# Kernel optimization log

Measured on AMD Instinct MI355X. Metric: run time of the kernel, lower is better.

Reference implementation:

```python
import jax, jax.numpy as jnp
import numpy as np

K_REP = 8
K_SMOOTH = 16
W_CHAMFER, W_REP, W_COV, W_SMOOTH = 1.0, 0.1, 0.2, 0.05
REP_THRESHOLD = 0.005


def setup_inputs() -> dict:
    key = jax.random.key(0)
    k1, k2, k3 = jax.random.split(key, 3)
    pred = jax.random.normal(k1, (4, 4096, 3), dtype=jnp.float32)
    gt = jax.random.normal(k2, (4, 4096, 3), dtype=jnp.float32)
    partial = jax.random.normal(k3, (4, 2048, 3), dtype=jnp.float32)
    return {"pred": pred, "gt": gt, "partial": partial}


def pairwise_dist(a, b):
    # a: [B,M,3], b: [B,N,3] -> Euclidean distances [B,M,N] (torch.cdist)
    sq = (jnp.sum(a * a, -1)[:, :, None] + jnp.sum(b * b, -1)[:, None, :]
          - 2.0 * jnp.einsum('bmd,bnd->bmn', a, b))
    sq = jnp.maximum(sq, 0.0)
    safe = jnp.where(sq > 1e-12, sq, 1.0)  # avoid NaN grad of sqrt at 0
    return jnp.where(sq > 1e-12, jnp.sqrt(safe), 0.0)


def _forward(pred, gt, partial):
    B, N, _ = pred.shape
    # --- chamfer (mean of bidirectional nearest-neighbor distances) ---
    d_pg = pairwise_dist(pred, gt)  # [B,N,N]
    chamfer = (jnp.mean(jnp.min(d_pg, axis=2)) + jnp.mean(jnp.min(d_pg, axis=1))) * W_CHAMFER

    # shared pred-pred distance matrix for repulsion + smoothness
    d_pp = pairwise_dist(pred, pred)  # [B,N,N]

    # --- repulsion: k nearest (excluding self via +1e6 on diagonal) ---
    d_rep = d_pp + jnp.eye(N, dtype=d_pp.dtype) * 1e6
    neg_knn, _ = jax.lax.top_k(-d_rep, K_REP)  # smallest k distances
    knn_dist = -neg_knn
    repulsion = jnp.mean(jax.nn.relu(REP_THRESHOLD - knn_dist)) * W_REP

    # --- smoothness: variance of centered kNN neighborhoods (self included) ---
    _, knn_idx = jax.lax.top_k(-d_pp, K_SMOOTH)  # [B,N,k]
    neighbors = pred[jnp.arange(B)[:, None, None], knn_idx]  # [B,N,k,3]
    center = jnp.mean(neighbors, axis=2, keepdims=True)
    dev = neighbors - center
    # torch .var() over all k*3 elements, unbiased (ddof=1); mean(dev)==0
    var = jnp.sum(dev * dev, axis=(2, 3)) / (K_SMOOTH * 3 - 1)  # [B,N]
    smoothness = jnp.mean(var) * W_SMOOTH

    # --- coverage: per-sample masked mean of min dist partial->pred ---
    mask = (jnp.sum(jnp.abs(partial), axis=-1) > 1e-6).astype(pred.dtype)  # [B,Np]
    d_cp = pairwise_dist(partial, pred)  # [B,Np,N]
    min_dist = jnp.min(d_cp, axis=-1)  # [B,Np]
    cnt = jnp.sum(mask, axis=-1)  # [B]
    per_b = jnp.where(cnt > 0, jnp.sum(min_dist * mask, axis=-1) / jnp.maximum(cnt, 1.0), 0.0)
    coverage = jnp.mean(per_b) * W_COV  # == sum_b(...) / B

    total = chamfer + repulsion + coverage + smoothness
    return jnp.stack([chamfer, repulsion, coverage, smoothness, total])


def reference(pred, gt, partial):
    return _forward(pred, gt, partial)
```

## Files before the change

kernel.cpp:

```cpp
#include <hip/hip_runtime.h>
#include <math.h>

#define BB 4
#define NN 4096
#define MP 2048

__device__ __forceinline__ unsigned med3u(unsigned a, unsigned b, unsigned c) {
    unsigned d;
    asm("v_med3_u32 %0, %1, %2, %3" : "=v"(d) : "v"(a), "v"(b), "v"(c));
    return d;
}

template <int K>
__device__ __forceinline__ void insertK(unsigned (&keys)[K], unsigned key) {
#pragma unroll
    for (int k = K - 1; k >= 1; --k)
        keys[k] = med3u(key, keys[k - 1], keys[k]);
    keys[0] = min(key, keys[0]);
}

template <int K>
__device__ __forceinline__ void insertK_if(unsigned (&keys)[K], unsigned key) {
    if (key < keys[K - 1]) insertK<K>(keys, key);
}

__global__ __launch_bounds__(256) void kfused(const float* __restrict__ pred,
                                              const float* __restrict__ gt,
                                              const float* __restrict__ partial,
                                              float* __restrict__ wrowc,
                                              float* __restrict__ wcolc,
                                              float* __restrict__ wcovc,
                                              unsigned* __restrict__ wkeys) {
    constexpr int NCH = 32, CAND = 128;
    constexpr int NCHM = 8, CANDM = 512;
    constexpr int KPB = 4 * 8 * NCH;
    constexpr int RPB = 4 * 8 * NCHM;
    constexpr int R1 = KPB + RPB;
    constexpr int R2 = R1 + RPB;
    __shared__ float4 cand[CANDM];
    int bid = blockIdx.x;
    int t = threadIdx.x;

    if (bid < KPB) {
        int b = bid >> 8; int r = bid & 255;
        int qb = r >> 5; int ch = r & 31;
        if (t < CAND) {
            int j = ch * CAND + t;
            const float* p = pred + ((size_t)b * NN + j) * 3;
            float x = p[0], y = p[1], z = p[2];
            cand[t] = make_float4(x, y, z, fmaf(z, z, fmaf(y, y, x * x)));
        }
        __syncthreads();
        int i0 = qb * 512 + t;
        int i1 = i0 + 256;
        const float* q0 = pred + ((size_t)b * NN + i0) * 3;
        const float* q1 = pred + ((size_t)b * NN + i1) * 3;
        float a0x = -2.f * q0[0], a0y = -2.f * q0[1], a0z = -2.f * q0[2];
        float a1x = -2.f * q1[0], a1y = -2.f * q1[1], a1z = -2.f * q1[2];
        float q0q = fmaf(q0[2], q0[2], fmaf(q0[1], q0[1], q0[0] * q0[0]));
        float q1q = fmaf(q1[2], q1[2], fmaf(q1[1], q1[1], q1[0] * q1[0]));
        unsigned keysA[4], keysB[4];
#pragma unroll
        for (int k = 0; k < 4; ++k) { keysA[k] = 0xFFFFFFFFu; keysB[k] = 0xFFFFFFFFu; }
        unsigned jbase = (unsigned)(ch * CAND);
#pragma unroll 8
        for (int jj = 0; jj < CAND; ++jj) {
            float4 c = cand[jj];
            float s0 = fmaf(a0z, c.z, fmaf(a0y, c.y, fmaf(a0x, c.x, q0q + c.w)));
            float s1 = fmaf(a1z, c.z, fmaf(a1y, c.y, fmaf(a1x, c.x, q1q + c.w)));
            s0 = fmaxf(s0, 0.f);
            s1 = fmaxf(s1, 0.f);
            unsigned idn = jbase + (unsigned)jj;
            insertK<4>(keysA, (__float_as_uint(s0) & 0xFFFFF000u) | idn);
            insertK<4>(keysB, (__float_as_uint(s1) & 0xFFFFF000u) | idn);
        }
        ((uint4*)wkeys)[((size_t)b * NN + i0) * NCH + ch] =
            make_uint4(keysA[0], keysA[1], keysA[2], keysA[3]);
        ((uint4*)wkeys)[((size_t)b * NN + i1) * NCH + ch] =
            make_uint4(keysB[0], keysB[1], keysB[2], keysB[3]);
    } else {
        const float* qptr; const float* cptr; float* outp;
        int b, qb, ch, qn;
        if (bid < R1) {
            int l = bid - KPB;
            b = l >> 6; int r = l & 63; qb = r >> 3; ch = r & 7;
            qptr = pred; cptr = gt; outp = wrowc; qn = NN;
        } else if (bid < R2) {
            int l = bid - R1;
            b = l >> 6; int r = l & 63; qb = r >> 3; ch = r & 7;
            qptr = gt; cptr = pred; outp = wcolc; qn = NN;
        } else {
            int l = bid - R2;
            b = l >> 5; int r = l & 31; qb = r >> 3; ch = r & 7;
            qptr = partial; cptr = pred; outp = wcovc; qn = MP;
        }
        for (int s = t; s < CANDM; s += 256) {
            int j = ch * CANDM + s;
            const float* p = cptr + ((size_t)b * NN + j) * 3;
            float x = p[0], y = p[1], z = p[2];
            cand[s] = make_float4(x, y, z, fmaf(z, z, fmaf(y, y, x * x)));
        }
        __syncthreads();
        int i0 = qb * 512 + t;
        int i1 = i0 + 256;
        const float* q0 = qptr + ((size_t)b * qn + i0) * 3;
        const float* q1 = qptr + ((size_t)b * qn + i1) * 3;
        float a0x = -2.f * q0[0], a0y = -2.f * q0[1], a0z = -2.f * q0[2];
        float a1x = -2.f * q1[0], a1y = -2.f * q1[1], a1z = -2.f * q1[2];
        float q0q = fmaf(q0[2], q0[2], fmaf(q0[1], q0[1], q0[0] * q0[0]));
        float q1q = fmaf(q1[2], q1[2], fmaf(q1[1], q1[1], q1[0] * q1[0]));
        float m0 = 1e30f, m1 = 1e30f;
#pragma unroll 8
        for (int jj = 0; jj < CANDM; ++jj) {
            float4 c = cand[jj];
            float s0 = fmaf(a0z, c.z, fmaf(a0y, c.y, fmaf(a0x, c.x, q0q + c.w)));
            float s1 = fmaf(a1z, c.z, fmaf(a1y, c.y, fmaf(a1x, c.x, q1q + c.w)));
            m0 = fminf(m0, s0);
            m1 = fminf(m1, s1);
        }
        outp[(size_t)ch * (4 * qn) + (size_t)b * qn + i0] = fmaxf(m0, 0.f);
        outp[(size_t)ch * (4 * qn) + (size_t)b * qn + i1] = fmaxf(m1, 0.f);
    }
}

__global__ __launch_bounds__(256) void kmid2(const float* __restrict__ pred,
                                             const unsigned* __restrict__ wkeys,
                                             const float* __restrict__ wrowc,
                                             const float* __restrict__ wcolc,
                                             const float* __restrict__ wcovc,
                                             const float* __restrict__ partialpts,
                                             float2* __restrict__ partialsB,
                                             float2* __restrict__ partials2) {
    constexpr int NCH = 32;
    constexpr int NCHM = 8;
    __shared__ float ra[4], rb[4];
    int bid = blockIdx.x;
    int t = threadIdx.x;

    if (bid < 64) {
        int q = bid * 256 + t;
        int b = q >> 12;
        int i = q & (NN - 1);
        unsigned keys[16];
#pragma unroll
        for (int k = 0; k < 16; ++k) keys[k] = 0xFFFFFFFFu;
        const uint4* src = (const uint4*)(wkeys + (size_t)q * (NCH * 4));
#pragma unroll 1
        for (int lb = 0; lb < NCH; lb += 8) {
            uint4 h[8];
#pragma unroll
            for (int u = 0; u < 8; ++u) h[u] = src[lb + u];
#pragma unroll
            for (int u = 0; u < 8; ++u) {
                uint4 k4 = h[u];
                if (k4.x < keys[15]) {
                    insertK<16>(keys, k4.x);
                    insertK_if<16>(keys, k4.y);
                    insertK_if<16>(keys, k4.z);
                    insertK_if<16>(keys, k4.w);
                }
            }
        }
        const float* qp = pred + ((size_t)b * NN + i) * 3;
        float qx = qp[0], qy = qp[1], qz = qp[2];
        float qq = fmaf(qz, qz, fmaf(qy, qy, qx * qx));
        float cxv[16], cyv[16], czv[16];
#pragma unroll
        for (int r = 0; r < 16; ++r) {
            int idx = (int)(keys[r] & 0xFFFu);
            const float* p = pred + ((size_t)b * NN + idx) * 3;
            cxv[r] = p[0]; cyv[r] = p[1]; czv[r] = p[2];
        }
        float rep = 0.f;
#pragma unroll
        for (int r = 1; r <= 8; ++r) {
            float x = cxv[r], y = cyv[r], z = czv[r];
            float bb2 = fmaf(z, z, fmaf(y, y, x * x));
            float dot = fmaf(qz, z, fmaf(qy, y, qx * x));
            float sq  = fmaxf(fmaf(-2.f, dot, qq + bb2), 0.f);
            float d = (sq > 1e-12f) ? sqrtf(sq) : 0.f;
            rep += fmaxf(0.005f - d, 0.f);
        }
        float sx = 0.f, sy = 0.f, sz = 0.f;
#pragma unroll
        for (int r = 0; r < 16; ++r) { sx += cxv[r]; sy += cyv[r]; sz += czv[r]; }
        float mx = sx * (1.f / 16.f), my = sy * (1.f / 16.f), mz = sz * (1.f / 16.f);
        float var = 0.f;
#pragma unroll
        for (int r = 0; r < 16; ++r) {
            float dx = cxv[r] - mx, dy = cyv[r] - my, dz = czv[r] - mz;
            var += dx * dx + dy * dy + dz * dz;
        }
        var *= (1.f / 47.f);
#pragma unroll
        for (int off = 32; off > 0; off >>= 1) {
            rep += __shfl_down(rep, off);
            var += __shfl_down(var, off);
        }
        int wid = t >> 6, lane = t & 63;
        if (lane == 0) { ra[wid] = rep; rb[wid] = var; }
        __syncthreads();
        if (t == 0)
            partialsB[bid] = make_float2(ra[0] + ra[1] + ra[2] + ra[3],
                                         rb[0] + rb[1] + rb[2] + rb[3]);
    } else {
        int bid2 = bid - 64;
        float pa = 0.f, pb = 0.f;
        if (bid2 < 64) {
            int q = bid2 * 256 + t;
            float m = 1e30f;
#pragma unroll
            for (int ch = 0; ch < NCHM; ++ch)
                m = fminf(m, wrowc[(size_t)ch * (BB * NN) + q]);
            pa = (m > 1e-12f) ? sqrtf(m) : 0.f;
        } else if (bid2 < 128) {
            int q = (bid2 - 64) * 256 + t;
            float m = 1e30f;
#pragma unroll
            for (int ch = 0; ch < NCHM; ++ch)
                m = fminf(m, wcolc[(size_t)ch * (BB * NN) + q]);
            pa = (m > 1e-12f) ? sqrtf(m) : 0.f;
        } else {
            int q = (bid2 - 128) * 256 + t;
            float m = 1e30f;
#pragma unroll
            for (int ch = 0; ch < NCHM; ++ch)
                m = fminf(m, wcovc[(size_t)ch * (BB * MP) + q]);
            const float* p = partialpts + (size_t)q * 3;
            float am = fabsf(p[0]) + fabsf(p[1]) + fabsf(p[2]);
            float msk = (am > 1e-6f) ? 1.f : 0.f;
            float d = (m > 1e-12f) ? sqrtf(m) : 0.f;
            pa = d * msk; pb = msk;
        }
#pragma unroll
        for (int off = 32; off > 0; off >>= 1) {
            pa += __shfl_down(pa, off);
            pb += __shfl_down(pb, off);
        }
        int wid = t >> 6, lane = t & 63;
        if (lane == 0) { ra[wid] = pa; rb[wid] = pb; }
        __syncthreads();
        if (t == 0)
            partials2[bid2] = make_float2(ra[0] + ra[1] + ra[2] + ra[3],
                                          rb[0] + rb[1] + rb[2] + rb[3]);
    }
}

__global__ __launch_bounds__(256) void kfinal2(const float2* __restrict__ partials2,
                                               const float2* __restrict__ partialsB,
                                               float* __restrict__ out) {
    __shared__ float lds[12];
    int t = threadIdx.x;
    int wid = t >> 6, lane = t & 63;
    if (wid == 0) {
        float v = partials2[lane].x;
#pragma unroll
        for (int off = 32; off > 0; off >>= 1) v += __shfl_down(v, off);
        if (lane == 0) lds[0] = v;
    } else if (wid == 1) {
        float v = partials2[64 + lane].x;
#pragma unroll
        for (int off = 32; off > 0; off >>= 1) v += __shfl_down(v, off);
        if (lane == 0) lds[1] = v;
    } else if (wid == 2) {
        float ss = 0.f, cc = 0.f;
        if (lane < 32) { float2 p = partials2[128 + lane]; ss = p.x; cc = p.y; }
#pragma unroll
        for (int off = 4; off > 0; off >>= 1) {
            ss += __shfl_down(ss, off, 8);
            cc += __shfl_down(cc, off, 8);
        }
        if (lane < 32 && (lane & 7) == 0) {
            int bb = lane >> 3;
            lds[4 + 2 * bb] = ss;
            lds[5 + 2 * bb] = cc;
        }
    } else {
        float2 p0 = partialsB[lane];
        float rep = p0.x, var = p0.y;
#pragma unroll
        for (int off = 32; off > 0; off >>= 1) {
            rep += __shfl_down(rep, off);
            var += __shfl_down(var, off);
        }
        if (lane == 0) { lds[2] = rep; lds[3] = var; }
    }
    __syncthreads();
    if (t == 0) {
        const float inv_bn = 1.f / (float)(BB * NN);
        float chamfer = (lds[0] + lds[1]) * inv_bn;
        float repulsion = lds[2] * inv_bn * (1.f / 8.f) * 0.1f;
        float cov = 0.f;
#pragma unroll
        for (int bb = 0; bb < 4; ++bb) {
            float cs = lds[4 + 2 * bb], cc = lds[5 + 2 * bb];
            cov += (cc > 0.f) ? cs / fmaxf(cc, 1.f) : 0.f;
        }
        float coverage = cov * 0.25f * 0.2f;
        float smooth = lds[3] * inv_bn * 0.05f;
        out[0] = chamfer;
        out[1] = repulsion;
        out[2] = coverage;
        out[3] = smooth;
        out[4] = chamfer + repulsion + coverage + smooth;
    }
}

extern "C" void kernel_launch(void* const* d_in, const int* in_sizes, int n_in,
                              void* d_out, int out_size, void* d_ws, size_t ws_size,
                              hipStream_t stream) {
    const float* pred    = (const float*)d_in[0];
    const float* gt      = (const float*)d_in[1];
    const float* partial = (const float*)d_in[2];
    float* out = (float*)d_out;

    const size_t NQ = (size_t)BB * NN;
    const size_t NC = (size_t)BB * MP;

    unsigned* wkeys = (unsigned*)d_ws;
    float* wrowc = (float*)(wkeys + NQ * 128);
    float* wcolc = wrowc + 8 * NQ;
    float* wcovc = wcolc + 8 * NQ;
    float2* pB = (float2*)(wcovc + 8 * NC);
    float2* p2 = pB + 64;

    kfused<<<1664, 256, 0, stream>>>(pred, gt, partial, wrowc, wcolc, wcovc, wkeys);
    kmid2<<<224, 256, 0, stream>>>(pred, wkeys, wrowc, wcolc, wcovc, partial, pB, p2);
    kfinal2<<<1, 256, 0, stream>>>(p2, pB, out);
}
```

Before: 55.24 us.

## Fuse final reduction into mid kernel via last-block atomic counter, halve block size

Removes the separate single-block final reduction launch by having the last-finishing block of the mid kernel, detected through an atomic counter reset in the first kernel, perform the final combine and write the output. The mid kernel also moves from 256-thread to 128-thread blocks, doubling the block count to spread the top-k merge work across more CUs. The intent is to save one kernel launch and its dependency gap and to raise parallelism in the small mid stage. In exchange it adds threadfences and an atomic per block, and correctness relies on the counter being reset by the earlier kernel on the same stream.

```diff
diff --git a/kernel.cpp b/kernel.cpp
--- a/kernel.cpp
+++ b/kernel.cpp
@@ -30,7 +30,8 @@
                                               float* __restrict__ wrowc,
                                               float* __restrict__ wcolc,
                                               float* __restrict__ wcovc,
-                                              unsigned* __restrict__ wkeys) {
+                                              unsigned* __restrict__ wkeys,
+                                              unsigned* __restrict__ counter) {
     constexpr int NCH = 32, CAND = 128;
     constexpr int NCHM = 8, CANDM = 512;
     constexpr int KPB = 4 * 8 * NCH;
@@ -40,6 +41,7 @@
     __shared__ float4 cand[CANDM];
     int bid = blockIdx.x;
     int t = threadIdx.x;
+    if (bid == 0 && t == 0) *counter = 0;
 
     if (bid < KPB) {
         int b = bid >> 8; int r = bid & 255;
@@ -123,22 +125,27 @@
     }
 }
 
-__global__ __launch_bounds__(256) void kmid2(const float* __restrict__ pred,
+__global__ __launch_bounds__(128) void kmid2(const float* __restrict__ pred,
                                              const unsigned* __restrict__ wkeys,
                                              const float* __restrict__ wrowc,
                                              const float* __restrict__ wcolc,
                                              const float* __restrict__ wcovc,
                                              const float* __restrict__ partialpts,
                                              float2* __restrict__ partialsB,
-                                             float2* __restrict__ partials2) {
+                                             float2* __restrict__ partials2,
+                                             unsigned* __restrict__ counter,
+                                             float* __restrict__ out) {
     constexpr int NCH = 32;
     constexpr int NCHM = 8;
-    __shared__ float ra[4], rb[4];
+    __shared__ float ra[2], rb[2];
+    __shared__ float lds[12];
+    __shared__ int is_last;
     int bid = blockIdx.x;
     int t = threadIdx.x;
-
-    if (bid < 64) {
-        int q = bid * 256 + t;
+    int wid = t >> 6, lane = t & 63;
+
+    if (bid < 128) {
+        int q = bid * 128 + t;
         int b = q >> 12;
         int i = q & (NN - 1);
         unsigned keys[16];
@@ -197,31 +204,28 @@
             rep += __shfl_down(rep, off);
             var += __shfl_down(var, off);
         }
-        int wid = t >> 6, lane = t & 63;
         if (lane == 0) { ra[wid] = rep; rb[wid] = var; }
         __syncthreads();
-        if (t == 0)
-            partialsB[bid] = make_float2(ra[0] + ra[1] + ra[2] + ra[3],
-                                         rb[0] + rb[1] + rb[2] + rb[3]);
+        if (t == 0) partialsB[bid] = make_float2(ra[0] + ra[1], rb[0] + rb[1]);
     } else {
-        int bid2 = bid - 64;
+        int bid2 = bid - 128;
         float pa = 0.f, pb = 0.f;
-        if (bid2 < 64) {
-            int q = bid2 * 256 + t;
+        if (bid2 < 128) {
+            int q = bid2 * 128 + t;
             float m = 1e30f;
 #pragma unroll
             for (int ch = 0; ch < NCHM; ++ch)
                 m = fminf(m, wrowc[(size_t)ch * (BB * NN) + q]);
             pa = (m > 1e-12f) ? sqrtf(m) : 0.f;
-        } else if (bid2 < 128) {
-            int q = (bid2 - 64) * 256 + t;
+        } else if (bid2 < 256) {
+            int q = (bid2 - 128) * 128 + t;
             float m = 1e30f;
 #pragma unroll
             for (int ch = 0; ch < NCHM; ++ch)
                 m = fminf(m, wcolc[(size_t)ch * (BB * NN) + q]);
             pa = (m > 1e-12f) ? sqrtf(m) : 0.f;
         } else {
-            int q = (bid2 - 128) * 256 + t;
+            int q = (bid2 - 256) * 128 + t;
             float m = 1e30f;
 #pragma unroll
             for (int ch = 0; ch < NCHM; ++ch)
@@ -237,47 +241,42 @@
             pa += __shfl_down(pa, off);
             pb += __shfl_down(pb, off);
         }
-        int wid = t >> 6, lane = t & 63;
         if (lane == 0) { ra[wid] = pa; rb[wid] = pb; }
         __syncthreads();
-        if (t == 0)
-            partials2[bid2] = make_float2(ra[0] + ra[1] + ra[2] + ra[3],
-                                          rb[0] + rb[1] + rb[2] + rb[3]);
+        if (t == 0) partials2[bid2] = make_float2(ra[0] + ra[1], rb[0] + rb[1]);
     }
-}
-
-__global__ __launch_bounds__(256) void kfinal2(const float2* __restrict__ partials2,
-                                               const float2* __restrict__ partialsB,
-                                               float* __restrict__ out) {
-    __shared__ float lds[12];
-    int t = threadIdx.x;
-    int wid = t >> 6, lane = t & 63;
+
+    __threadfence();
+    if (t == 0) is_last = (atomicAdd(counter, 1u) == 447u);
+    __syncthreads();
+    if (!is_last) return;
+    __threadfence();
+
     if (wid == 0) {
-        float v = partials2[lane].x;
-#pragma unroll
-        for (int off = 32; off > 0; off >>= 1) v += __shfl_down(v, off);
-        if (lane == 0) lds[0] = v;
-    } else if (wid == 1) {
-        float v = partials2[64 + lane].x;
-#pragma unroll
-        for (int off = 32; off > 0; off >>= 1) v += __shfl_down(v, off);
-        if (lane == 0) lds[1] = v;
-    } else if (wid == 2) {
-        float ss = 0.f, cc = 0.f;
-        if (lane < 32) { float2 p = partials2[128 + lane]; ss = p.x; cc = p.y; }
-#pragma unroll
-        for (int off = 4; off > 0; off >>= 1) {
-            ss += __shfl_down(ss, off, 8);
-            cc += __shfl_down(cc, off, 8);
-        }
-        if (lane < 32 && (lane & 7) == 0) {
-            int bb = lane >> 3;
+        float sr = partials2[lane].x + partials2[64 + lane].x;
+#pragma unroll
+        for (int off = 32; off > 0; off >>= 1) sr += __shfl_down(sr, off);
+        if (lane == 0) lds[0] = sr;
+        float sc = partials2[128 + lane].x + partials2[192 + lane].x;
+#pragma unroll
+        for (int off = 32; off > 0; off >>= 1) sc += __shfl_down(sc, off);
+        if (lane == 0) lds[1] = sc;
+    } else {
+        float2 pc = partials2[256 + lane];
+        float ss = pc.x, cc = pc.y;
+#pragma unroll
+        for (int off = 8; off > 0; off >>= 1) {
+            ss += __shfl_down(ss, off, 16);
+            cc += __shfl_down(cc, off, 16);
+        }
+        if ((lane & 15) == 0) {
+            int bb = lane >> 4;
             lds[4 + 2 * bb] = ss;
             lds[5 + 2 * bb] = cc;
         }
-    } else {
         float2 p0 = partialsB[lane];
-        float rep = p0.x, var = p0.y;
+        float2 p1 = partialsB[64 + lane];
+        float rep = p0.x + p1.x, var = p0.y + p1.y;
 #pragma unroll
         for (int off = 32; off > 0; off >>= 1) {
             rep += __shfl_down(rep, off);
@@ -322,9 +321,11 @@
     float* wcolc = wrowc + 8 * NQ;
     float* wcovc = wcolc + 8 * NQ;
     float2* pB = (float2*)(wcovc + 8 * NC);
-    float2* p2 = pB + 64;
-
-    kfused<<<1664, 256, 0, stream>>>(pred, gt, partial, wrowc, wcolc, wcovc, wkeys);
-    kmid2<<<224, 256, 0, stream>>>(pred, wkeys, wrowc, wcolc, wcovc, partial, pB, p2);
-    kfinal2<<<1, 256, 0, stream>>>(p2, pB, out);
-}
+    float2* p2 = pB + 128;
+    unsigned* counter = (unsigned*)(p2 + 320);
+
+    kfused<<<1664, 256, 0, stream>>>(pred, gt, partial, wrowc, wcolc, wcovc,
+                                     wkeys, counter);
+    kmid2<<<448, 128, 0, stream>>>(pred, wkeys, wrowc, wcolc, wcovc, partial,
+                                   pB, p2, counter, out);
+}
```

New measurement: 67.67 us (median of 2 runs). +22.5%, slower.
